# Kernel optimization log

Measured on AMD Instinct MI355X. Metric: run time of the kernel, lower is better.

Reference implementation:

```python
import jax, jax.numpy as jnp
import numpy as np

SD, MD, HM, HR, N_STEPS = 64, 64, 128, 128, 10
N_VARS, DEG = 2048, 8


def _build_graph():
    rng = np.random.default_rng(0)
    n = N_VARS
    us = np.repeat(np.arange(n), 4)
    ks = np.tile(np.arange(1, 5), n)
    vs = (us + ks) % n
    factors = np.stack([np.minimum(us, vs), np.maximum(us, vs)], 1)  # [F,2], u<v
    F = factors.shape[0]
    J = np.zeros((n, n), np.float32)
    vals = rng.normal(size=F).astype(np.float32)
    J[factors[:, 0], factors[:, 1]] = vals
    J[factors[:, 1], factors[:, 0]] = vals
    b = rng.normal(size=n).astype(np.float32)
    var_node = factors.reshape(-1)          # variable of each message node
    fac_node = np.repeat(np.arange(F), 2)   # factor of each message node
    M = var_node.shape[0]
    order = np.argsort(var_node, kind='stable').reshape(n, DEG)
    jj = np.broadcast_to(order[:, :, None], (n, DEG, DEG))
    ii = np.broadcast_to(order[:, None, :], (n, DEG, DEG))
    mask = fac_node[jj] != fac_node[ii]     # same variable, different factor
    f2v_row = jj[mask].astype(np.int64)
    f2v_col = ii[mask].astype(np.int64)
    fu = fac_node[f2v_row]; fv = fac_node[f2v_col]
    feat5 = np.stack([b[var_node[f2v_col]],
                      J[factors[fu, 0], factors[fu, 1]], J[factors[fu, 1], factors[fu, 0]],
                      J[factors[fv, 0], factors[fv, 1]], J[factors[fv, 1], factors[fv, 0]]], 1).astype(np.float32)
    v2f_row = np.arange(M, dtype=np.int64)
    v2f_col = v2f_row ^ 1                   # same factor, other variable
    f = fac_node[v2f_row]
    feat4 = np.stack([b[var_node[v2f_row]], b[var_node[v2f_col]],
                      J[factors[f, 0], factors[f, 1]], J[factors[f, 1], factors[f, 0]]], 1).astype(np.float32)
    return f2v_row, f2v_col, feat5, v2f_row, v2f_col, feat4, var_node.astype(np.int64), M


def setup_inputs():
    f2v_row, f2v_col, feat5, v2f_row, v2f_col, feat4, readout_col, M = _build_graph()
    rng = np.random.default_rng(1)
    def lin(o, i):
        return rng.normal(0, 0.1, size=(o, i)).astype(np.float32), np.zeros(o, np.float32)
    def gru_p():
        s = 1.0 / np.sqrt(SD)
        return tuple(rng.uniform(-s, s, sh).astype(np.float32)
                     for sh in ((3 * SD, MD), (3 * SD, SD), (3 * SD,), (3 * SD,)))
    d = {}
    d['attn_W'], d['attn_b'] = lin(1, 2 * SD)
    d['v2f_W1'], d['v2f_b1'] = lin(HM, 2 * SD + 5)
    d['v2f_W2'], d['v2f_b2'] = lin(HM, HM)
    d['v2f_W3'], d['v2f_b3'] = lin(MD, HM)
    d['f2v_W1'], d['f2v_b1'] = lin(HM, 2 * SD + 4)
    d['f2v_W2'], d['f2v_b2'] = lin(HM, HM)
    d['f2v_W3'], d['f2v_b3'] = lin(MD, HM)
    d['ro_W1'], d['ro_b1'] = lin(HR, SD)
    d['ro_W2'], d['ro_b2'] = lin(HR, HR)
    d['ro_W3'], d['ro_b3'] = lin(2, HR)
    d['gv_Wi'], d['gv_Wh'], d['gv_bi'], d['gv_bh'] = gru_p()
    d['gf_Wi'], d['gf_Wh'], d['gf_bi'], d['gf_bh'] = gru_p()
    d = {k: jnp.asarray(v) for k, v in d.items()}
    d.update(feat5=jnp.asarray(feat5), feat4=jnp.asarray(feat4),
             f2v_row=jnp.asarray(f2v_row), f2v_col=jnp.asarray(f2v_col),
             v2f_row=jnp.asarray(v2f_row), v2f_col=jnp.asarray(v2f_col),
             readout_col=jnp.asarray(readout_col), n_vars=N_VARS, n_msg=int(M))
    return d


def _mlp3(x, W1, b1, W2, b2, W3, b3):
    h = jax.nn.relu(x @ W1.T + b1)
    h = jax.nn.relu(h @ W2.T + b2)
    return h @ W3.T + b3


def _gru(x, h, Wi, Wh, bi, bh):
    gi = x @ Wi.T + bi
    gh = h @ Wh.T + bh
    ir, iz, in_ = jnp.split(gi, 3, -1)
    hr, hz, hn = jnp.split(gh, 3, -1)
    r = jax.nn.sigmoid(ir + hr)
    z = jax.nn.sigmoid(iz + hz)
    n = jnp.tanh(in_ + r * hn)
    return (1.0 - z) * n + z * h


def reference(attn_W, attn_b, v2f_W1, v2f_b1, v2f_W2, v2f_b2, v2f_W3, v2f_b3,
              f2v_W1, f2v_b1, f2v_W2, f2v_b2, f2v_W3, f2v_b3,
              ro_W1, ro_b1, ro_W2, ro_b2, ro_W3, ro_b3,
              gv_Wi, gv_Wh, gv_bi, gv_bh, gf_Wi, gf_Wh, gf_bi, gf_bh,
              feat5, feat4, f2v_row, f2v_col, v2f_row, v2f_col, readout_col, n_vars, n_msg):
    v2f_h = jnp.zeros((n_msg, SD), feat5.dtype)
    f2v_h = jnp.zeros((n_msg, SD), feat5.dtype)

    def attn(hi, hj):
        e = jax.nn.leaky_relu(jnp.concatenate([hi, hj], -1) @ attn_W.T + attn_b)
        return jax.nn.softmax(e, axis=0)  # global softmax over all edges, shape [E,1]

    for _ in range(N_STEPS):
        hi = f2v_h[f2v_row]; hj = v2f_h[f2v_col]
        msg = _mlp3(jnp.concatenate([hi, hj, feat5], -1),
                    v2f_W1, v2f_b1, v2f_W2, v2f_b2, v2f_W3, v2f_b3) * attn(hi, hj)
        v2f_h = _gru(jax.ops.segment_sum(msg, f2v_col, num_segments=n_msg),
                     v2f_h, gv_Wi, gv_Wh, gv_bi, gv_bh)
        hi = v2f_h[v2f_row]; hj = f2v_h[v2f_col]
        msg = _mlp3(jnp.concatenate([hi, hj, feat4], -1),
                    f2v_W1, f2v_b1, f2v_W2, f2v_b2, f2v_W3, f2v_b3) * attn(hi, hj)
        f2v_h = _gru(jax.ops.segment_sum(msg, v2f_col, num_segments=n_msg),
                     f2v_h, gf_Wi, gf_Wh, gf_bi, gf_bh)

    node = jax.ops.segment_sum(f2v_h, readout_col, num_segments=n_vars)
    return jax.nn.softmax(_mlp3(node, ro_W1, ro_b1, ro_W2, ro_b2, ro_W3, ro_b3), axis=1)
```

## Files before the change

### kernel.cpp

```cpp
#include <hip/hip_runtime.h>
#include <cstdint>
#include <cstddef>

#define E1C 114688
#define MMC 16384
#define NVC 2048
#define NSTEPS 10

typedef __bf16 bf16x8 __attribute__((ext_vector_type(8)));
typedef float  f32x4  __attribute__((ext_vector_type(4)));

__device__ __forceinline__ float sigm(float x) { return 1.0f / (1.0f + expf(-x)); }
__device__ __forceinline__ bf16x8 ld8(const __bf16* p) {
  return *reinterpret_cast<const bf16x8*>(p);
}

#define NJOBS 13
struct PrepJobs {
  const float* src[NJOBS];
  __bf16* dst0;
  int kin[NJOBS];
  int nin[NJOBS];
  int ntile[NJOBS];
  int base[NJOBS];
  int total;
};

__global__ __launch_bounds__(256) void k_prep_all(PrepJobs J) {
  int gid = blockIdx.x * 256 + threadIdx.x;
  if (gid >= J.total) return;
  int jb = 0;
  #pragma unroll
  for (int x = 1; x < NJOBS; ++x) if (gid >= J.base[x]) jb = x;
  int d = gid - J.base[jb];
  int group = d >> 9, rr = d & 511, ln = rr >> 3, j = rr & 7;
  int q = ln >> 4, m16 = ln & 15;
  int NT = J.ntile[jb];
  int kc = group / NT, nt = group - kc * NT;
  int n = nt * 16 + m16, k = kc * 32 + q * 8 + j;
  int kin = J.kin[jb];
  float v = (k < kin && n < J.nin[jb]) ? J.src[jb][(size_t)n * kin + k] : 0.f;
  J.dst0[gid] = (__bf16)v;
}

template<int FDIM, int EPB, int MODE>
__global__ __launch_bounds__(256, 3) void k_mlp(
    const float* __restrict__ hA, const float* __restrict__ hB,
    const int* __restrict__ rowIdx, const int* __restrict__ colIdx,
    const float* __restrict__ feat,
    const __bf16* __restrict__ W1f, const float* __restrict__ b1,
    const __bf16* __restrict__ W2f, const float* __restrict__ b2,
    const __bf16* __restrict__ W3f, const float* __restrict__ b3,
    const float* __restrict__ attnW, const float* __restrict__ attnB,
    float* __restrict__ xout, float* __restrict__ Zpart)
{
  constexpr int RPW = EPB / 4;
  constexpr int MTILES = EPB / 16;
  constexpr int LPE = (EPB == 112) ? 2 : 4;
  constexpr int ACT = RPW * LPE;
  constexpr int ND = 128 / LPE;
  __shared__ __align__(16) __bf16 Xs[EPB][168];
  __shared__ float wexp[EPB];
  __shared__ float zp[4];
  __shared__ int mloc[16];
  const int t = threadIdx.x, lane = t & 63, w = t >> 6;
  const int r0 = w * RPW;
  const int e0 = blockIdx.x * EPB;

  {
    const int half = lane >> 5, l2 = lane & 31;
    const float* hbase = half ? hB : hA;
    const int* ibase = half ? colIdx : rowIdx;
    #pragma unroll
    for (int i = 0; i < RPW; ++i) {
      int e = r0 + i;
      int idx = ibase[e0 + e];
      float2 v = *reinterpret_cast<const float2*>(hbase + (size_t)idx * 64 + l2 * 2);
      union { __bf16 b[2]; unsigned u; } cv;
      cv.b[0] = (__bf16)v.x; cv.b[1] = (__bf16)v.y;
      *reinterpret_cast<unsigned*>(&Xs[e][half * 64 + l2 * 2]) = cv.u;
    }
    #pragma unroll
    for (int it = 0; it < RPW / 2; ++it) {
      int e = r0 + it * 2 + (lane >> 5);
      int f = lane & 31;
      float fv = (f < FDIM) ? feat[(size_t)(e0 + e) * FDIM + f] : 0.f;
      Xs[e][128 + f] = (__bf16)fv;
    }
  }

  if (MODE == 0 && t < 16) {
    int v = blockIdx.x * 2 + (t >> 3), b = t & 7;
    mloc[t] = colIdx[v * 56 + (b == 0 ? 7 : b - 1)];
  }

  {
    int eL = r0 + lane / LPE, part = lane % LPE;
    bool act = (lane < ACT);
    float s = 0.f;
    if (act) {
      #pragma unroll
      for (int jj = 0; jj < ND / 8; ++jj) {
        bf16x8 xv = ld8(&Xs[eL][part * ND + jj * 8]);
        #pragma unroll
        for (int j = 0; j < 8; ++j) s += attnW[part * ND + jj * 8 + j] * (float)xv[j];
      }
    }
    s += __shfl_xor(s, 1);
    if (LPE == 4) s += __shfl_xor(s, 2);
    float ex = 0.f;
    if (act && part == 0) {
      float le = s + attnB[0];
      le = le > 0.f ? le : 0.01f * le;
      ex = expf(le);
      wexp[eL] = ex;
    }
    #pragma unroll
    for (int off = 1; off < 64; off <<= 1) ex += __shfl_xor(ex, off);
    if (lane == 0) zp[w] = ex;
  }
  __syncthreads();
  if (t == 0) Zpart[blockIdx.x] = zp[0] + zp[1] + zp[2] + zp[3];

  const int m16 = lane & 15, q = lane >> 4;

  {
    bf16x8 B0[5], B1[5];
    #pragma unroll
    for (int kc = 0; kc < 5; ++kc) {
      B0[kc] = ld8(W1f + (size_t)(kc * 8 + w * 2 + 0) * 512 + lane * 8);
      B1[kc] = ld8(W1f + (size_t)(kc * 8 + w * 2 + 1) * 512 + lane * 8);
    }
    f32x4 a0[MTILES], a1[MTILES];
    float bv0 = b1[(w * 2) * 16 + m16], bv1 = b1[(w * 2 + 1) * 16 + m16];
    #pragma unroll
    for (int mt = 0; mt < MTILES; ++mt) {
      a0[mt] = (f32x4){bv0, bv0, bv0, bv0};
      a1[mt] = (f32x4){bv1, bv1, bv1, bv1};
      #pragma unroll
      for (int kc = 0; kc < 5; ++kc) {
        bf16x8 av = ld8(&Xs[mt * 16 + m16][kc * 32 + q * 8]);
        a0[mt] = __builtin_amdgcn_mfma_f32_16x16x32_bf16(av, B0[kc], a0[mt], 0, 0, 0);
        a1[mt] = __builtin_amdgcn_mfma_f32_16x16x32_bf16(av, B1[kc], a1[mt], 0, 0, 0);
      }
    }
    __syncthreads();
    #pragma unroll
    for (int mt = 0; mt < MTILES; ++mt)
      #pragma unroll
      for (int r2 = 0; r2 < 4; ++r2) {
        float v0 = a0[mt][r2]; v0 = v0 > 0.f ? v0 : 0.f;
        float v1 = a1[mt][r2]; v1 = v1 > 0.f ? v1 : 0.f;
        Xs[mt * 16 + q * 4 + r2][(w * 2) * 16 + m16]     = (__bf16)v0;
        Xs[mt * 16 + q * 4 + r2][(w * 2 + 1) * 16 + m16] = (__bf16)v1;
      }
    __syncthreads();
  }

  {
    bf16x8 B0[4], B1[4];
    #pragma unroll
    for (int kc = 0; kc < 4; ++kc) {
      B0[kc] = ld8(W2f + (size_t)(kc * 8 + w * 2 + 0) * 512 + lane * 8);
      B1[kc] = ld8(W2f + (size_t)(kc * 8 + w * 2 + 1) * 512 + lane * 8);
    }
    f32x4 a0[MTILES], a1[MTILES];
    float bv0 = b2[(w * 2) * 16 + m16], bv1 = b2[(w * 2 + 1) * 16 + m16];
    #pragma unroll
    for (int mt = 0; mt < MTILES; ++mt) {
      a0[mt] = (f32x4){bv0, bv0, bv0, bv0};
      a1[mt] = (f32x4){bv1, bv1, bv1, bv1};
      #pragma unroll
      for (int kc = 0; kc < 4; ++kc) {
        bf16x8 av = ld8(&Xs[mt * 16 + m16][kc * 32 + q * 8]);
        a0[mt] = __builtin_amdgcn_mfma_f32_16x16x32_bf16(av, B0[kc], a0[mt], 0, 0, 0);
        a1[mt] = __builtin_amdgcn_mfma_f32_16x16x32_bf16(av, B1[kc], a1[mt], 0, 0, 0);
      }
    }
    __syncthreads();
    #pragma unroll
    for (int mt = 0; mt < MTILES; ++mt)
      #pragma unroll
      for (int r2 = 0; r2 < 4; ++r2) {
        float v0 = a0[mt][r2]; v0 = v0 > 0.f ? v0 : 0.f;
        float v1 = a1[mt][r2]; v1 = v1 > 0.f ? v1 : 0.f;
        Xs[mt * 16 + q * 4 + r2][(w * 2) * 16 + m16]     = (__bf16)v0;
        Xs[mt * 16 + q * 4 + r2][(w * 2 + 1) * 16 + m16] = (__bf16)v1;
      }
    __syncthreads();
  }

  f32x4 a3[MTILES];
  {
    bf16x8 B3[4];
    #pragma unroll
    for (int kc = 0; kc < 4; ++kc)
      B3[kc] = ld8(W3f + (size_t)(kc * 4 + w) * 512 + lane * 8);
    float bv = b3[w * 16 + m16];
    #pragma unroll
    for (int mt = 0; mt < MTILES; ++mt) {
      a3[mt] = (f32x4){bv, bv, bv, bv};
      #pragma unroll
      for (int kc = 0; kc < 4; ++kc) {
        bf16x8 av = ld8(&Xs[mt * 16 + m16][kc * 32 + q * 8]);
        a3[mt] = __builtin_amdgcn_mfma_f32_16x16x32_bf16(av, B3[kc], a3[mt], 0, 0, 0);
      }
    }
  }
  __syncthreads();

  float* Ms = reinterpret_cast<float*>(&Xs[0][0]);
  #pragma unroll
  for (int mt = 0; mt < MTILES; ++mt)
    #pragma unroll
    for (int r2 = 0; r2 < 4; ++r2) {
      int e = mt * 16 + q * 4 + r2;
      Ms[e * 68 + w * 16 + m16] = wexp[e] * a3[mt][r2];
    }
  __syncthreads();

  if (MODE == 0) {
    int node = t >> 4, cg = t & 15;
    int vloc = node >> 3, b = node & 7;
    float4 s4 = make_float4(0.f, 0.f, 0.f, 0.f);
    #pragma unroll
    for (int a1 = 0; a1 < 7; ++a1) {
      int a = a1 + (a1 >= b ? 1 : 0);
      int e = vloc * 56 + a * 7 + b - (b > a ? 1 : 0);
      float4 mv = *reinterpret_cast<const float4*>(Ms + e * 68 + cg * 4);
      s4.x += mv.x; s4.y += mv.y; s4.z += mv.z; s4.w += mv.w;
    }
    *reinterpret_cast<float4*>(xout + (size_t)mloc[node] * 64 + cg * 4) = s4;
  } else {
    #pragma unroll
    for (int it = 0; it < 4; ++it) {
      int idx = t + it * 256;
      int ml = idx >> 4, cg = idx & 15;
      float4 v = *reinterpret_cast<const float4*>(Ms + (ml ^ 1) * 68 + cg * 4);
      *reinterpret_cast<float4*>(xout + (size_t)(e0 + ml) * 64 + cg * 4) = v;
    }
  }
}

__global__ __launch_bounds__(256) void k_gru(
    const float* __restrict__ xt, const float* __restrict__ Zp, int zn,
    float* __restrict__ hbuf,
    const __bf16* __restrict__ WiF, const __bf16* __restrict__ WhF,
    const float* __restrict__ bi, const float* __restrict__ bh)
{
  __shared__ __align__(16) __bf16 xsf[4096];
  __shared__ __align__(16) __bf16 hsf[4096];
  __shared__ float hs32[64][68];
  __shared__ float zred[4];
  const int t = threadIdx.x, lane = t & 63, w = t >> 6;
  const int n0 = blockIdx.x * 64;

  {
    float zs = 0.f;
    for (int i = t; i < zn; i += 256) zs += Zp[i];
    #pragma unroll
    for (int off = 32; off; off >>= 1) zs += __shfl_down(zs, off);
    if (lane == 0) zred[w] = zs;
  }
  __syncthreads();
  const float invZ = 1.0f / (zred[0] + zred[1] + zred[2] + zred[3]);

  {
    const int i = t >> 2, cb = t & 3;
    const float4* xp = (const float4*)(xt + (size_t)(n0 + i) * 64 + cb * 16);
    float4 x4[4] = {xp[0], xp[1], xp[2], xp[3]};
    #pragma unroll
    for (int k = 0; k < 4; ++k) {
      x4[k].x *= invZ; x4[k].y *= invZ; x4[k].z *= invZ; x4[k].w *= invZ;
    }
    const float* xf = (const float*)x4;
    #pragma unroll
    for (int half = 0; half < 2; ++half) {
      __bf16 v8[8];
      #pragma unroll
      for (int j = 0; j < 8; ++j) v8[j] = (__bf16)xf[half * 8 + j];
      int addr = (i >> 4) * 1024 + (cb >> 1) * 512 + ((cb & 1) * 2 + half) * 128 + (i & 15) * 8;
      *(uint4*)(xsf + addr) = *(const uint4*)v8;
    }
    const float4* hp = (const float4*)(hbuf + (size_t)(n0 + i) * 64 + cb * 16);
    float4 h4[4] = {hp[0], hp[1], hp[2], hp[3]};
    *(float4*)(&hs32[i][cb * 16 + 0])  = h4[0];
    *(float4*)(&hs32[i][cb * 16 + 4])  = h4[1];
    *(float4*)(&hs32[i][cb * 16 + 8])  = h4[2];
    *(float4*)(&hs32[i][cb * 16 + 12]) = h4[3];
    const float* hf = (const float*)h4;
    #pragma unroll
    for (int half = 0; half < 2; ++half) {
      __bf16 v8[8];
      #pragma unroll
      for (int j = 0; j < 8; ++j) v8[j] = (__bf16)hf[half * 8 + j];
      int addr = (i >> 4) * 1024 + (cb >> 1) * 512 + ((cb & 1) * 2 + half) * 128 + (i & 15) * 8;
      *(uint4*)(hsf + addr) = *(const uint4*)v8;
    }
  }
  __syncthreads();

  const int m16 = lane & 15, q = lane >> 4;
  f32x4 gi[12], gh[12];
  #pragma unroll
  for (int nt = 0; nt < 12; ++nt) { gi[nt] = (f32x4){0,0,0,0}; gh[nt] = (f32x4){0,0,0,0}; }
  #pragma unroll
  for (int kc = 0; kc < 2; ++kc) {
    bf16x8 ax = ld8(xsf + w * 1024 + kc * 512 + lane * 8);
    bf16x8 ah = ld8(hsf + w * 1024 + kc * 512 + lane * 8);
    #pragma unroll
    for (int nt = 0; nt < 12; ++nt) {
      bf16x8 bx = ld8(WiF + (size_t)(kc * 12 + nt) * 512 + lane * 8);
      gi[nt] = __builtin_amdgcn_mfma_f32_16x16x32_bf16(ax, bx, gi[nt], 0, 0, 0);
      bf16x8 bh8 = ld8(WhF + (size_t)(kc * 12 + nt) * 512 + lane * 8);
      gh[nt] = __builtin_amdgcn_mfma_f32_16x16x32_bf16(ah, bh8, gh[nt], 0, 0, 0);
    }
  }

  #pragma unroll
  for (int nt = 0; nt < 4; ++nt) {
    int o = nt * 16 + m16;
    float bir = bi[o]       + bh[o];
    float biz = bi[64 + o]  + bh[64 + o];
    float bin = bi[128 + o], bhn = bh[128 + o];
    #pragma unroll
    for (int r = 0; r < 4; ++r) {
      int nl = w * 16 + q * 4 + r;
      float rg = sigm(gi[nt][r]     + gh[nt][r]     + bir);
      float zg = sigm(gi[nt + 4][r] + gh[nt + 4][r] + biz);
      float ng = tanhf(gi[nt + 8][r] + bin + rg * (gh[nt + 8][r] + bhn));
      float ho = hs32[nl][o];
      hbuf[(size_t)(n0 + nl) * 64 + o] = (1.f - zg) * ng + zg * ho;
    }
  }
}

__global__ __launch_bounds__(256) void k_readout(
    const float* __restrict__ f2v_h, const int* __restrict__ f2v_col,
    const __bf16* __restrict__ W1f, const float* __restrict__ b1,
    const __bf16* __restrict__ W2f, const float* __restrict__ b2,
    const __bf16* __restrict__ W3f, const float* __restrict__ b3,
    float* __restrict__ out)
{
  __shared__ __align__(16) __bf16 Xs[64][136];
  const int t = threadIdx.x, lane = t & 63, w = t >> 6;
  const int r0 = w * 16;
  const int v0 = blockIdx.x * 64;

  #pragma unroll
  for (int i = 0; i < 16; ++i) {
    int v = v0 + r0 + i;
    float s = 0.f;
    #pragma unroll
    for (int b = 0; b < 8; ++b) {
      int m = f2v_col[v * 56 + (b == 0 ? 7 : (b - 1))];
      s += f2v_h[(size_t)m * 64 + lane];
    }
    Xs[r0 + i][lane] = (__bf16)s;
  }

  const int m16 = lane & 15, q = lane >> 4;

  {
    f32x4 acc[8];
    #pragma unroll
    for (int nt = 0; nt < 8; ++nt) {
      float bv = b1[nt * 16 + m16];
      acc[nt] = (f32x4){bv, bv, bv, bv};
    }
    #pragma unroll
    for (int kc = 0; kc < 2; ++kc) {
      bf16x8 av = ld8(&Xs[r0 + m16][kc * 32 + q * 8]);
      #pragma unroll
      for (int nt = 0; nt < 8; ++nt) {
        bf16x8 bv = ld8(W1f + (size_t)(kc * 8 + nt) * 512 + lane * 8);
        acc[nt] = __builtin_amdgcn_mfma_f32_16x16x32_bf16(av, bv, acc[nt], 0, 0, 0);
      }
    }
    #pragma unroll
    for (int nt = 0; nt < 8; ++nt)
      #pragma unroll
      for (int r2 = 0; r2 < 4; ++r2) {
        float v = acc[nt][r2]; v = v > 0.f ? v : 0.f;
        Xs[r0 + q * 4 + r2][nt * 16 + m16] = (__bf16)v;
      }
  }

  {
    f32x4 acc[8];
    #pragma unroll
    for (int nt = 0; nt < 8; ++nt) {
      float bv = b2[nt * 16 + m16];
      acc[nt] = (f32x4){bv, bv, bv, bv};
    }
    #pragma unroll
    for (int kc = 0; kc < 4; ++kc) {
      bf16x8 av = ld8(&Xs[r0 + m16][kc * 32 + q * 8]);
      #pragma unroll
      for (int nt = 0; nt < 8; ++nt) {
        bf16x8 bv = ld8(W2f + (size_t)(kc * 8 + nt) * 512 + lane * 8);
        acc[nt] = __builtin_amdgcn_mfma_f32_16x16x32_bf16(av, bv, acc[nt], 0, 0, 0);
      }
    }
    #pragma unroll
    for (int nt = 0; nt < 8; ++nt)
      #pragma unroll
      for (int r2 = 0; r2 < 4; ++r2) {
        float v = acc[nt][r2]; v = v > 0.f ? v : 0.f;
        Xs[r0 + q * 4 + r2][nt * 16 + m16] = (__bf16)v;
      }
  }

  {
    f32x4 acc = (f32x4){0, 0, 0, 0};
    if (m16 < 2) { float bv = b3[m16]; acc = (f32x4){bv, bv, bv, bv}; }
    #pragma unroll
    for (int kc = 0; kc < 4; ++kc) {
      bf16x8 av = ld8(&Xs[r0 + m16][kc * 32 + q * 8]);
      bf16x8 bv = ld8(W3f + (size_t)kc * 512 + lane * 8);
      acc = __builtin_amdgcn_mfma_f32_16x16x32_bf16(av, bv, acc, 0, 0, 0);
    }
    #pragma unroll
    for (int r = 0; r < 4; ++r) {
      float other = __shfl_xor(acc[r], 1);
      if (m16 == 0) {
        float l0 = acc[r], l1 = other;
        float mx = fmaxf(l0, l1);
        float p0 = expf(l0 - mx), p1 = expf(l1 - mx);
        float inv = 1.0f / (p0 + p1);
        int v = v0 + r0 + q * 4 + r;
        *reinterpret_cast<float2*>(out + (size_t)v * 2) = make_float2(p0 * inv, p1 * inv);
      }
    }
  }
}

extern "C" void kernel_launch(void* const* d_in, const int* in_sizes, int n_in,
                              void* d_out, int out_size, void* d_ws, size_t ws_size,
                              hipStream_t stream) {
  const float* attn_W = (const float*)d_in[0];
  const float* attn_b = (const float*)d_in[1];
  const float* v2f_W1 = (const float*)d_in[2];
  const float* v2f_b1 = (const float*)d_in[3];
  const float* v2f_W2 = (const float*)d_in[4];
  const float* v2f_b2 = (const float*)d_in[5];
  const float* v2f_W3 = (const float*)d_in[6];
  const float* v2f_b3 = (const float*)d_in[7];
  const float* f2v_W1 = (const float*)d_in[8];
  const float* f2v_b1 = (const float*)d_in[9];
  const float* f2v_W2 = (const float*)d_in[10];
  const float* f2v_b2 = (const float*)d_in[11];
  const float* f2v_W3 = (const float*)d_in[12];
  const float* f2v_b3 = (const float*)d_in[13];
  const float* ro_W1  = (const float*)d_in[14];
  const float* ro_b1  = (const float*)d_in[15];
  const float* ro_W2  = (const float*)d_in[16];
  const float* ro_b2  = (const float*)d_in[17];
  const float* ro_W3  = (const float*)d_in[18];
  const float* ro_b3  = (const float*)d_in[19];
  const float* gv_Wi  = (const float*)d_in[20];
  const float* gv_Wh  = (const float*)d_in[21];
  const float* gv_bi  = (const float*)d_in[22];
  const float* gv_bh  = (const float*)d_in[23];
  const float* gf_Wi  = (const float*)d_in[24];
  const float* gf_Wh  = (const float*)d_in[25];
  const float* gf_bi  = (const float*)d_in[26];
  const float* gf_bh  = (const float*)d_in[27];
  const float* feat5  = (const float*)d_in[28];
  const float* feat4  = (const float*)d_in[29];
  const int* f2v_row  = (const int*)d_in[30];
  const int* f2v_col  = (const int*)d_in[31];
  const int* v2f_row  = (const int*)d_in[32];
  const int* v2f_col  = (const int*)d_in[33];

  float* ws = (float*)d_ws;
  float* xt1    = ws;
  float* xt2    = xt1 + (size_t)MMC * 64;
  float* h_v2f  = xt2 + (size_t)MMC * 64;
  float* h_f2v  = h_v2f + (size_t)MMC * 64;
  float* Zp     = h_f2v + (size_t)MMC * 64;
  __bf16* wbuf  = (__bf16*)(((uintptr_t)(Zp + 20 * 1024) + 15) & ~(uintptr_t)15);
  __bf16* w1v = wbuf;
  __bf16* w2v = w1v + 20480;
  __bf16* w3v = w2v + 16384;
  __bf16* w1f = w3v + 8192;
  __bf16* w2f = w1f + 20480;
  __bf16* w3f = w2f + 16384;
  __bf16* wiv = w3f + 8192;
  __bf16* whv = wiv + 12288;
  __bf16* wif = whv + 12288;
  __bf16* whf = wif + 12288;
  __bf16* wr1 = whf + 12288;
  __bf16* wr2 = wr1 + 8192;
  __bf16* wr3 = wr2 + 16384;

  hipMemsetAsync(h_v2f, 0, (size_t)2 * MMC * 64 * sizeof(float), stream);

  {
    PrepJobs J;
    const float* srcs[NJOBS] = {v2f_W1, v2f_W2, v2f_W3, f2v_W1, f2v_W2, f2v_W3,
                                gv_Wi, gv_Wh, gf_Wi, gf_Wh, ro_W1, ro_W2, ro_W3};
    int kin[NJOBS]  = {133, 128, 128, 132, 128, 128, 64, 64, 64, 64, 64, 128, 128};
    int nin[NJOBS]  = {128, 128, 64, 128, 128, 64, 192, 192, 192, 192, 128, 128, 2};
    int nt[NJOBS]   = {8, 8, 4, 8, 8, 4, 12, 12, 12, 12, 8, 8, 1};
    int size[NJOBS] = {20480, 16384, 8192, 20480, 16384, 8192,
                       12288, 12288, 12288, 12288, 8192, 16384, 2048};
    int cum = 0;
    for (int i = 0; i < NJOBS; ++i) {
      J.src[i] = srcs[i]; J.kin[i] = kin[i]; J.nin[i] = nin[i]; J.ntile[i] = nt[i];
      J.base[i] = cum; cum += size[i];
    }
    J.dst0 = wbuf; J.total = cum;
    k_prep_all<<<(cum + 255) / 256, 256, 0, stream>>>(J);
  }

  const int ZN1 = E1C / 112;
  const int ZN2 = MMC / 64;

  for (int s = 0; s < NSTEPS; ++s) {
    float* z1 = Zp + (size_t)(s * 2) * 1024;
    float* z2 = Zp + (size_t)(s * 2 + 1) * 1024;
    k_mlp<5, 112, 0><<<E1C / 112, 256, 0, stream>>>(
        h_f2v, h_v2f, f2v_row, f2v_col, feat5,
        w1v, v2f_b1, w2v, v2f_b2, w3v, v2f_b3,
        attn_W, attn_b, xt1, z1);
    k_gru<<<MMC / 64, 256, 0, stream>>>(xt1, z1, ZN1, h_v2f,
                                        wiv, whv, gv_bi, gv_bh);
    k_mlp<4, 64, 1><<<MMC / 64, 256, 0, stream>>>(
        h_v2f, h_f2v, v2f_row, v2f_col, feat4,
        w1f, f2v_b1, w2f, f2v_b2, w3f, f2v_b3,
        attn_W, attn_b, xt2, z2);
    k_gru<<<MMC / 64, 256, 0, stream>>>(xt2, z2, ZN2, h_f2v,
                                        wif, whf, gf_bi, gf_bh);
  }
  k_readout<<<NVC / 64, 256, 0, stream>>>(h_f2v, f2v_col,
                                          wr1, ro_b1, wr2, ro_b2, wr3, ro_b3,
                                          (float*)d_out);
}
```

Before: 682.6 us.

## Fuse v2f GRU update with f2v message MLP into one kernel

Adds a kernel that performs the v2f GRU update for a 64-row block and then immediately computes the f2v message MLP, attention weights and pairwise-swap scatter for the same rows. The new h_v2f rows stay in shared memory as bf16 instead of being written and re-read by a separate launch. This is valid because v2f_row is the identity and v2f_col is row^1, so each block only needs its own rows. It removes one launch per step and a global round-trip of the hidden state, at the cost of higher register and shared-memory pressure (launch bounds of 3 blocks per SM).

```diff
diff --git a/kernel.cpp b/kernel.cpp
--- a/kernel.cpp
+++ b/kernel.cpp
@@ -239,6 +239,261 @@
       float4 v = *reinterpret_cast<const float4*>(Ms + (ml ^ 1) * 68 + cg * 4);
       *reinterpret_cast<float4*>(xout + (size_t)(e0 + ml) * 64 + cg * 4) = v;
     }
+  }
+}
+
+__global__ __launch_bounds__(256, 3) void k_fuse2(
+    const float* __restrict__ xt, const float* __restrict__ Zp, int zn,
+    float* __restrict__ hbuf,
+    const float* __restrict__ hOther,
+    const float* __restrict__ feat,
+    const __bf16* __restrict__ WiF, const __bf16* __restrict__ WhF,
+    const float* __restrict__ bi, const float* __restrict__ bh,
+    const __bf16* __restrict__ W1f, const float* __restrict__ b1,
+    const __bf16* __restrict__ W2f, const float* __restrict__ b2,
+    const __bf16* __restrict__ W3f, const float* __restrict__ b3,
+    const float* __restrict__ attnW, const float* __restrict__ attnB,
+    float* __restrict__ xout, float* __restrict__ Zpart2)
+{
+  __shared__ __align__(16) char smem[34880];
+  __bf16* xsf = (__bf16*)smem;
+  __bf16* hsf = (__bf16*)(smem + 8192);
+  float (*hs32)[68] = (float (*)[68])(smem + 16384);
+  __bf16 (*Xs)[168] = (__bf16 (*)[168])smem;
+  float* wexp = (float*)(smem + 33792);
+  float* zred = (float*)(smem + 34048);
+  float* zp   = (float*)(smem + 34064);
+  const int t = threadIdx.x, lane = t & 63, w = t >> 6;
+  const int n0 = blockIdx.x * 64;
+  const int m16 = lane & 15, q = lane >> 4;
+
+  {
+    float zs = 0.f;
+    for (int i = t; i < zn; i += 256) zs += Zp[i];
+    #pragma unroll
+    for (int off = 32; off; off >>= 1) zs += __shfl_down(zs, off);
+    if (lane == 0) zred[w] = zs;
+  }
+  __syncthreads();
+  const float invZ = 1.0f / (zred[0] + zred[1] + zred[2] + zred[3]);
+
+  {
+    const int i = t >> 2, cb = t & 3;
+    const float4* xp = (const float4*)(xt + (size_t)(n0 + i) * 64 + cb * 16);
+    float4 x4[4] = {xp[0], xp[1], xp[2], xp[3]};
+    #pragma unroll
+    for (int k = 0; k < 4; ++k) {
+      x4[k].x *= invZ; x4[k].y *= invZ; x4[k].z *= invZ; x4[k].w *= invZ;
+    }
+    const float* xf = (const float*)x4;
+    #pragma unroll
+    for (int half = 0; half < 2; ++half) {
+      __bf16 v8[8];
+      #pragma unroll
+      for (int j = 0; j < 8; ++j) v8[j] = (__bf16)xf[half * 8 + j];
+      int addr = (i >> 4) * 1024 + (cb >> 1) * 512 + ((cb & 1) * 2 + half) * 128 + (i & 15) * 8;
+      *(uint4*)(xsf + addr) = *(const uint4*)v8;
+    }
+    const float4* hp = (const float4*)(hbuf + (size_t)(n0 + i) * 64 + cb * 16);
+    float4 h4[4] = {hp[0], hp[1], hp[2], hp[3]};
+    *(float4*)(&hs32[i][cb * 16 + 0])  = h4[0];
+    *(float4*)(&hs32[i][cb * 16 + 4])  = h4[1];
+    *(float4*)(&hs32[i][cb * 16 + 8])  = h4[2];
+    *(float4*)(&hs32[i][cb * 16 + 12]) = h4[3];
+    const float* hf = (const float*)h4;
+    #pragma unroll
+    for (int half = 0; half < 2; ++half) {
+      __bf16 v8[8];
+      #pragma unroll
+      for (int j = 0; j < 8; ++j) v8[j] = (__bf16)hf[half * 8 + j];
+      int addr = (i >> 4) * 1024 + (cb >> 1) * 512 + ((cb & 1) * 2 + half) * 128 + (i & 15) * 8;
+      *(uint4*)(hsf + addr) = *(const uint4*)v8;
+    }
+  }
+  __syncthreads();
+
+  f32x4 gi[12], gh[12];
+  #pragma unroll
+  for (int nt = 0; nt < 12; ++nt) { gi[nt] = (f32x4){0,0,0,0}; gh[nt] = (f32x4){0,0,0,0}; }
+  #pragma unroll
+  for (int kc = 0; kc < 2; ++kc) {
+    bf16x8 ax = ld8(xsf + w * 1024 + kc * 512 + lane * 8);
+    bf16x8 ah = ld8(hsf + w * 1024 + kc * 512 + lane * 8);
+    #pragma unroll
+    for (int nt = 0; nt < 12; ++nt) {
+      bf16x8 bx = ld8(WiF + (size_t)(kc * 12 + nt) * 512 + lane * 8);
+      gi[nt] = __builtin_amdgcn_mfma_f32_16x16x32_bf16(ax, bx, gi[nt], 0, 0, 0);
+      bf16x8 bh8 = ld8(WhF + (size_t)(kc * 12 + nt) * 512 + lane * 8);
+      gh[nt] = __builtin_amdgcn_mfma_f32_16x16x32_bf16(ah, bh8, gh[nt], 0, 0, 0);
+    }
+  }
+
+  float resv[4][4];
+  #pragma unroll
+  for (int nt = 0; nt < 4; ++nt) {
+    int o = nt * 16 + m16;
+    float bir = bi[o]       + bh[o];
+    float biz = bi[64 + o]  + bh[64 + o];
+    float bin = bi[128 + o], bhn = bh[128 + o];
+    #pragma unroll
+    for (int r = 0; r < 4; ++r) {
+      int nl = w * 16 + q * 4 + r;
+      float rg = sigm(gi[nt][r]     + gh[nt][r]     + bir);
+      float zg = sigm(gi[nt + 4][r] + gh[nt + 4][r] + biz);
+      float ng = tanhf(gi[nt + 8][r] + bin + rg * (gh[nt + 8][r] + bhn));
+      float ho = hs32[nl][o];
+      float res = (1.f - zg) * ng + zg * ho;
+      resv[nt][r] = res;
+      hbuf[(size_t)(n0 + nl) * 64 + o] = res;
+    }
+  }
+  __syncthreads();
+
+  #pragma unroll
+  for (int nt = 0; nt < 4; ++nt)
+    #pragma unroll
+    for (int r = 0; r < 4; ++r)
+      Xs[w * 16 + q * 4 + r][nt * 16 + m16] = (__bf16)resv[nt][r];
+  {
+    const int half = lane >> 5, l2 = lane & 31;
+    #pragma unroll
+    for (int i = 0; i < 16; ++i) {
+      int e = w * 16 + i;
+      if (half == 0) {
+        float2 v = *reinterpret_cast<const float2*>(hOther + (size_t)((n0 + e) ^ 1) * 64 + l2 * 2);
+        union { __bf16 b[2]; unsigned u; } cv;
+        cv.b[0] = (__bf16)v.x; cv.b[1] = (__bf16)v.y;
+        *reinterpret_cast<unsigned*>(&Xs[e][64 + l2 * 2]) = cv.u;
+      } else {
+        float fv = (l2 < 4) ? feat[(size_t)(n0 + e) * 4 + l2] : 0.f;
+        Xs[e][128 + l2] = (__bf16)fv;
+      }
+    }
+  }
+
+  {
+    int eL = w * 16 + (lane >> 2), part = lane & 3;
+    float s = 0.f;
+    #pragma unroll
+    for (int jj = 0; jj < 4; ++jj) {
+      bf16x8 xv = ld8(&Xs[eL][part * 32 + jj * 8]);
+      #pragma unroll
+      for (int j = 0; j < 8; ++j) s += attnW[part * 32 + jj * 8 + j] * (float)xv[j];
+    }
+    s += __shfl_xor(s, 1); s += __shfl_xor(s, 2);
+    float ex = 0.f;
+    if (part == 0) {
+      float le = s + attnB[0];
+      le = le > 0.f ? le : 0.01f * le;
+      ex = expf(le);
+      wexp[eL] = ex;
+    }
+    #pragma unroll
+    for (int off = 1; off < 64; off <<= 1) ex += __shfl_xor(ex, off);
+    if (lane == 0) zp[w] = ex;
+  }
+  __syncthreads();
+  if (t == 0) Zpart2[blockIdx.x] = zp[0] + zp[1] + zp[2] + zp[3];
+
+  {
+    bf16x8 B0[5], B1[5];
+    #pragma unroll
+    for (int kc = 0; kc < 5; ++kc) {
+      B0[kc] = ld8(W1f + (size_t)(kc * 8 + w * 2 + 0) * 512 + lane * 8);
+      B1[kc] = ld8(W1f + (size_t)(kc * 8 + w * 2 + 1) * 512 + lane * 8);
+    }
+    f32x4 a0[4], a1[4];
+    float bv0 = b1[(w * 2) * 16 + m16], bv1 = b1[(w * 2 + 1) * 16 + m16];
+    #pragma unroll
+    for (int mt = 0; mt < 4; ++mt) {
+      a0[mt] = (f32x4){bv0, bv0, bv0, bv0};
+      a1[mt] = (f32x4){bv1, bv1, bv1, bv1};
+      #pragma unroll
+      for (int kc = 0; kc < 5; ++kc) {
+        bf16x8 av = ld8(&Xs[mt * 16 + m16][kc * 32 + q * 8]);
+        a0[mt] = __builtin_amdgcn_mfma_f32_16x16x32_bf16(av, B0[kc], a0[mt], 0, 0, 0);
+        a1[mt] = __builtin_amdgcn_mfma_f32_16x16x32_bf16(av, B1[kc], a1[mt], 0, 0, 0);
+      }
+    }
+    __syncthreads();
+    #pragma unroll
+    for (int mt = 0; mt < 4; ++mt)
+      #pragma unroll
+      for (int r2 = 0; r2 < 4; ++r2) {
+        float v0 = a0[mt][r2]; v0 = v0 > 0.f ? v0 : 0.f;
+        float v1 = a1[mt][r2]; v1 = v1 > 0.f ? v1 : 0.f;
+        Xs[mt * 16 + q * 4 + r2][(w * 2) * 16 + m16]     = (__bf16)v0;
+        Xs[mt * 16 + q * 4 + r2][(w * 2 + 1) * 16 + m16] = (__bf16)v1;
+      }
+    __syncthreads();
+  }
+
+  {
+    bf16x8 B0[4], B1[4];
+    #pragma unroll
+    for (int kc = 0; kc < 4; ++kc) {
+      B0[kc] = ld8(W2f + (size_t)(kc * 8 + w * 2 + 0) * 512 + lane * 8);
+      B1[kc] = ld8(W2f + (size_t)(kc * 8 + w * 2 + 1) * 512 + lane * 8);
+    }
+    f32x4 a0[4], a1[4];
+    float bv0 = b2[(w * 2) * 16 + m16], bv1 = b2[(w * 2 + 1) * 16 + m16];
+    #pragma unroll
+    for (int mt = 0; mt < 4; ++mt) {
+      a0[mt] = (f32x4){bv0, bv0, bv0, bv0};
+      a1[mt] = (f32x4){bv1, bv1, bv1, bv1};
+      #pragma unroll
+      for (int kc = 0; kc < 4; ++kc) {
+        bf16x8 av = ld8(&Xs[mt * 16 + m16][kc * 32 + q * 8]);
+        a0[mt] = __builtin_amdgcn_mfma_f32_16x16x32_bf16(av, B0[kc], a0[mt], 0, 0, 0);
+        a1[mt] = __builtin_amdgcn_mfma_f32_16x16x32_bf16(av, B1[kc], a1[mt], 0, 0, 0);
+      }
+    }
+    __syncthreads();
+    #pragma unroll
+    for (int mt = 0; mt < 4; ++mt)
+      #pragma unroll
+      for (int r2 = 0; r2 < 4; ++r2) {
+        float v0 = a0[mt][r2]; v0 = v0 > 0.f ? v0 : 0.f;
+        float v1 = a1[mt][r2]; v1 = v1 > 0.f ? v1 : 0.f;
+        Xs[mt * 16 + q * 4 + r2][(w * 2) * 16 + m16]     = (__bf16)v0;
+        Xs[mt * 16 + q * 4 + r2][(w * 2 + 1) * 16 + m16] = (__bf16)v1;
+      }
+    __syncthreads();
+  }
+
+  f32x4 a3[4];
+  {
+    bf16x8 B3[4];
+    #pragma unroll
+    for (int kc = 0; kc < 4; ++kc)
+      B3[kc] = ld8(W3f + (size_t)(kc * 4 + w) * 512 + lane * 8);
+    float bv = b3[w * 16 + m16];
+    #pragma unroll
+    for (int mt = 0; mt < 4; ++mt) {
+      a3[mt] = (f32x4){bv, bv, bv, bv};
+      #pragma unroll
+      for (int kc = 0; kc < 4; ++kc) {
+        bf16x8 av = ld8(&Xs[mt * 16 + m16][kc * 32 + q * 8]);
+        a3[mt] = __builtin_amdgcn_mfma_f32_16x16x32_bf16(av, B3[kc], a3[mt], 0, 0, 0);
+      }
+    }
+  }
+  __syncthreads();
+  float* Ms = reinterpret_cast<float*>(&Xs[0][0]);
+  #pragma unroll
+  for (int mt = 0; mt < 4; ++mt)
+    #pragma unroll
+    for (int r2 = 0; r2 < 4; ++r2) {
+      int e = mt * 16 + q * 4 + r2;
+      Ms[e * 68 + w * 16 + m16] = wexp[e] * a3[mt][r2];
+    }
+  __syncthreads();
+  #pragma unroll
+  for (int it = 0; it < 4; ++it) {
+    int idx = t + it * 256;
+    int ml = idx >> 4, cg = idx & 15;
+    float4 v = *reinterpret_cast<const float4*>(Ms + (ml ^ 1) * 68 + cg * 4);
+    *reinterpret_cast<float4*>(xout + (size_t)(n0 + ml) * 64 + cg * 4) = v;
   }
 }
 
@@ -524,10 +779,9 @@
         h_f2v, h_v2f, f2v_row, f2v_col, feat5,
         w1v, v2f_b1, w2v, v2f_b2, w3v, v2f_b3,
         attn_W, attn_b, xt1, z1);
-    k_gru<<<MMC / 64, 256, 0, stream>>>(xt1, z1, ZN1, h_v2f,
-                                        wiv, whv, gv_bi, gv_bh);
-    k_mlp<4, 64, 1><<<MMC / 64, 256, 0, stream>>>(
-        h_v2f, h_f2v, v2f_row, v2f_col, feat4,
+    k_fuse2<<<MMC / 64, 256, 0, stream>>>(
+        xt1, z1, ZN1, h_v2f, h_f2v, feat4,
+        wiv, whv, gv_bi, gv_bh,
         w1f, f2v_b1, w2f, f2v_b2, w3f, f2v_b3,
         attn_W, attn_b, xt2, z2);
     k_gru<<<MMC / 64, 256, 0, stream>>>(xt2, z2, ZN2, h_f2v,
```

Measured after the change: 701.3 us. 1.03x slower.
